# Kernel tuning notes

Measured on AMD Instinct MI355X. Metric: run time of the kernel, lower is better.

The kernel has to match this reference:

```python
import jax, jax.numpy as jnp
import numpy as np

MINVAL = 0.0
MAXVAL = 1.0
G = 4096   # grid_dim
C = 8      # channels
N = 4      # batch


def setup_inputs() -> dict:
    key = jax.random.key(0)
    k1, k2 = jax.random.split(key)
    # uniform 1-D grid on [0, 1) -> dx = 1/G (get_dx(grid))
    grid = jnp.arange(G, dtype=jnp.float32) / G
    density = jax.random.normal(k1, (N, 1, G), dtype=jnp.float32)
    # nn.Parameter xi initialized with nn.init.uniform_ -> U[0, 1)
    xi = jax.random.uniform(k2, (C,), dtype=jnp.float32)
    return {"density": density, "xi": xi, "grid": grid}


def reference(density, xi, grid):
    # density: (N, 1, G); xi: (C,); grid: (G,)
    dx = grid[1] - grid[0]                                   # uniform spacing
    g = jnp.abs(grid[:, None] - grid[None, :])               # (G, G) pairwise |x_i - x_j|
    xi_eff = 1.0 / (MINVAL + (MAXVAL - MINVAL) * jax.nn.sigmoid(xi))  # (C,)
    expo = jnp.exp(-g[None, :, :] * xi_eff[:, None, None])   # (C, G, G) dense kernel
    # 'i, jkl, ilm -> jim': sum over singleton channel k of density and grid dim l
    integral = jnp.einsum('i,jkl,ilm->jim', 0.5 * xi_eff, density, expo)  # (N, C, G)
    return integral * dx
```

## Files before the change

### kernel.cpp

```cpp
#include <hip/hip_runtime.h>


#define GG 4096
#define CC 8
#define NN 4
#define SS 16
#define SEG (GG / SS)
#define BLOCK 256
#define NCOMBO (NN * CC)
#define NBLK (NCOMBO * SS)

__global__ __launch_bounds__(BLOCK) void gconv_part(const float* __restrict__ density,
                                                    const float* __restrict__ xi,
                                                    const float* __restrict__ grid,
                                                    float* __restrict__ ws) {
    const int bid   = blockIdx.x;
    const int seg   = bid & (SS - 1);
    const int combo = bid >> 4;
    const int c     = combo & (CC - 1);
    const int n     = combo >> 3;
    const int tid   = threadIdx.x;
    const int g     = seg * SEG + tid;

    const float k  = 1.0f + expf(-xi[c]);
    const float x  = grid[g];
    const float d  = density[n * GG + g];
    const float xk = x * k;
    float sA = d * expf(xk);
    float sB = d * expf(-xk);

#pragma unroll
    for (int off = 32; off > 0; off >>= 1) {
        sA += __shfl_xor(sA, off, 64);
        sB += __shfl_xor(sB, off, 64);
    }
    __shared__ float wA[BLOCK / 64], wB[BLOCK / 64];
    const int wave = tid >> 6;
    if ((tid & 63) == 0) { wA[wave] = sA; wB[wave] = sB; }
    __syncthreads();
    if (tid == 0) {
        ws[bid]        = wA[0] + wA[1] + wA[2] + wA[3];
        ws[NBLK + bid] = wB[0] + wB[1] + wB[2] + wB[3];
    }
}

__global__ __launch_bounds__(BLOCK) void gconv_out(const float* __restrict__ density,
                                                   const float* __restrict__ xi,
                                                   const float* __restrict__ grid,
                                                   const float* __restrict__ ws,
                                                   float* __restrict__ out) {
    const int bid   = blockIdx.x;
    const int seg   = bid & (SS - 1);
    const int combo = bid >> 4;
    const int c     = combo & (CC - 1);
    const int n     = combo >> 3;
    const int tid   = threadIdx.x;
    const int lane  = tid & 63;
    const int wave  = tid >> 6;
    const int g     = seg * SEG + tid;

    const float k  = 1.0f + expf(-xi[c]);
    const float dx = grid[1] - grid[0];
    const float x  = grid[g];
    const float d  = density[n * GG + g];
    const float xk = x * k;
    const float ea = expf(xk);
    const float eb = expf(-xk);
    const float a  = d * ea;
    const float b  = d * eb;

    const float* TA = ws + combo * SS;
    const float* TB = ws + NBLK + combo * SS;
    float offA = 0.0f, offB = 0.0f;
#pragma unroll
    for (int s = 0; s < SS; ++s) {
        const float ta = TA[s];
        const float tb = TB[s];
        if (s < seg) offA += ta;
        if (s > seg) offB += tb;
    }

    float pa = a, sb = b;
#pragma unroll
    for (int off = 1; off < 64; off <<= 1) {
        const float tA = __shfl_up(pa, off, 64);
        if (lane >= off) pa += tA;
        const float tB = __shfl_down(sb, off, 64);
        if (lane + off < 64) sb += tB;
    }

    __shared__ float wTA[BLOCK / 64], wTB[BLOCK / 64];
    if (lane == 63) wTA[wave] = pa;
    if (lane == 0)  wTB[wave] = sb;
    __syncthreads();
    float wOffA = 0.0f, wOffB = 0.0f;
#pragma unroll
    for (int w = 0; w < BLOCK / 64; ++w) {
        if (w < wave) wOffA += wTA[w];
        if (w > wave) wOffB += wTB[w];
    }

    const float A = offA + wOffA + pa;
    const float B = offB + wOffB + (sb - b);
    const float scale = 0.5f * k * dx;
    out[(n * CC + c) * GG + g] = scale * (eb * A + ea * B);
}

extern "C" void kernel_launch(void* const* d_in, const int* in_sizes, int n_in,
                              void* d_out, int out_size, void* d_ws, size_t ws_size,
                              hipStream_t stream) {
    const float* density = (const float*)d_in[0];
    const float* xi      = (const float*)d_in[1];
    const float* grid    = (const float*)d_in[2];
    float* out           = (float*)d_out;
    float* ws            = (float*)d_ws;

    gconv_part<<<NBLK, BLOCK, 0, stream>>>(density, xi, grid, ws);
    gconv_out<<<NBLK, BLOCK, 0, stream>>>(density, xi, grid, ws, out);
}
```

Before: 60.68 us.

## Fuse segment-sum and output kernels by recomputing partial sums per block

Replaces the two-kernel scheme (per-segment partial sums in a workspace, then a scan kernel) with a single kernel. Each block recomputes the exp-weighted sums of all 16 segments of its density row and block-reduces them, so the second launch and the global workspace round trip go away. It also switches to the fast `__expf` intrinsic and rebuilds x from grid0 + l*dx instead of loading grid. The cost is about 16x redundant exp work and density reads per block. The rebuilt x assumes a uniform grid, and `__expf` may lose some precision.

```diff
diff --git a/kernel.cpp b/kernel.cpp
--- a/kernel.cpp
+++ b/kernel.cpp
@@ -7,47 +7,11 @@
 #define SS 16
 #define SEG (GG / SS)
 #define BLOCK 256
-#define NCOMBO (NN * CC)
-#define NBLK (NCOMBO * SS)
+#define NBLK (NN * CC * SS)
 
-__global__ __launch_bounds__(BLOCK) void gconv_part(const float* __restrict__ density,
-                                                    const float* __restrict__ xi,
-                                                    const float* __restrict__ grid,
-                                                    float* __restrict__ ws) {
-    const int bid   = blockIdx.x;
-    const int seg   = bid & (SS - 1);
-    const int combo = bid >> 4;
-    const int c     = combo & (CC - 1);
-    const int n     = combo >> 3;
-    const int tid   = threadIdx.x;
-    const int g     = seg * SEG + tid;
-
-    const float k  = 1.0f + expf(-xi[c]);
-    const float x  = grid[g];
-    const float d  = density[n * GG + g];
-    const float xk = x * k;
-    float sA = d * expf(xk);
-    float sB = d * expf(-xk);
-
-#pragma unroll
-    for (int off = 32; off > 0; off >>= 1) {
-        sA += __shfl_xor(sA, off, 64);
-        sB += __shfl_xor(sB, off, 64);
-    }
-    __shared__ float wA[BLOCK / 64], wB[BLOCK / 64];
-    const int wave = tid >> 6;
-    if ((tid & 63) == 0) { wA[wave] = sA; wB[wave] = sB; }
-    __syncthreads();
-    if (tid == 0) {
-        ws[bid]        = wA[0] + wA[1] + wA[2] + wA[3];
-        ws[NBLK + bid] = wB[0] + wB[1] + wB[2] + wB[3];
-    }
-}
-
-__global__ __launch_bounds__(BLOCK) void gconv_out(const float* __restrict__ density,
+__global__ __launch_bounds__(BLOCK) void gconv_one(const float* __restrict__ density,
                                                    const float* __restrict__ xi,
                                                    const float* __restrict__ grid,
-                                                   const float* __restrict__ ws,
                                                    float* __restrict__ out) {
     const int bid   = blockIdx.x;
     const int seg   = bid & (SS - 1);
@@ -57,30 +21,41 @@
     const int tid   = threadIdx.x;
     const int lane  = tid & 63;
     const int wave  = tid >> 6;
-    const int g     = seg * SEG + tid;
 
-    const float k  = 1.0f + expf(-xi[c]);
-    const float dx = grid[1] - grid[0];
-    const float x  = grid[g];
-    const float d  = density[n * GG + g];
-    const float xk = x * k;
-    const float ea = expf(xk);
-    const float eb = expf(-xk);
-    const float a  = d * ea;
-    const float b  = d * eb;
+    const float k     = 1.0f + __expf(-xi[c]);
+    const float grid0 = grid[0];
+    const float dx    = grid[1] - grid0;
+    const float* drow = density + n * GG;
 
-    const float* TA = ws + combo * SS;
-    const float* TB = ws + NBLK + combo * SS;
     float offA = 0.0f, offB = 0.0f;
+    float mya = 0.0f, myb = 0.0f, myea = 1.0f, myeb = 1.0f;
 #pragma unroll
-    for (int s = 0; s < SS; ++s) {
-        const float ta = TA[s];
-        const float tb = TB[s];
-        if (s < seg) offA += ta;
-        if (s > seg) offB += tb;
+    for (int i = 0; i < SS; ++i) {
+        const int l   = i * SEG + tid;
+        const float d = drow[l];
+        const float x = fmaf((float)l, dx, grid0);
+        const float ep = __expf(x * k);
+        const float em = __expf(-x * k);
+        const float a = d * ep;
+        const float b = d * em;
+        if (i < seg)      offA += a;
+        else if (i > seg) offB += b;
+        else { mya = a; myb = b; myea = ep; myeb = em; }
     }
 
-    float pa = a, sb = b;
+    float rA = offA, rB = offB;
+#pragma unroll
+    for (int off = 32; off > 0; off >>= 1) {
+        rA += __shfl_xor(rA, off, 64);
+        rB += __shfl_xor(rB, off, 64);
+    }
+    __shared__ float sRA[BLOCK / 64], sRB[BLOCK / 64];
+    if (lane == 0) { sRA[wave] = rA; sRB[wave] = rB; }
+    __syncthreads();
+    offA = sRA[0] + sRA[1] + sRA[2] + sRA[3];
+    offB = sRB[0] + sRB[1] + sRB[2] + sRB[3];
+
+    float pa = mya, sb = myb;
 #pragma unroll
     for (int off = 1; off < 64; off <<= 1) {
         const float tA = __shfl_up(pa, off, 64);
@@ -101,9 +76,9 @@
     }
 
     const float A = offA + wOffA + pa;
-    const float B = offB + wOffB + (sb - b);
+    const float B = offB + wOffB + (sb - myb);
     const float scale = 0.5f * k * dx;
-    out[(n * CC + c) * GG + g] = scale * (eb * A + ea * B);
+    out[combo * GG + seg * SEG + tid] = scale * (myeb * A + myea * B);
 }
 
 extern "C" void kernel_launch(void* const* d_in, const int* in_sizes, int n_in,
@@ -113,8 +88,6 @@
     const float* xi      = (const float*)d_in[1];
     const float* grid    = (const float*)d_in[2];
     float* out           = (float*)d_out;
-    float* ws            = (float*)d_ws;
 
-    gconv_part<<<NBLK, BLOCK, 0, stream>>>(density, xi, grid, ws);
-    gconv_out<<<NBLK, BLOCK, 0, stream>>>(density, xi, grid, ws, out);
+    gconv_one<<<NBLK, BLOCK, 0, stream>>>(density, xi, grid, out);
 }
```

Result: no change. 61.50 us (+1.4%).
